# Kernel optimization log

Hardware: AMD Instinct MI355X
Metric: run time of the kernel (lower is better)

Reference implementation:

```python
import jax, jax.numpy as jnp
import numpy as np

N_NODES = 50000
N_EDGES = 1600000
N_GRAPHS = 256
F_IN = 1080   # -> 536 -> 264 -> 128 after three (k=10, s=2) convs
HID = 128
OUT = 64


def setup_inputs() -> dict:
    key = jax.random.key(0)
    ks = jax.random.split(key, 12)
    def w(k, shape, fan):
        return (jax.random.normal(k, shape, jnp.float32) / np.sqrt(fan)).astype(jnp.float32)
    x = jax.random.normal(ks[0], (N_NODES, F_IN), jnp.float32)
    edge_index = jax.random.randint(ks[1], (2, N_EDGES), 0, N_NODES, dtype=jnp.int32)
    batch = jnp.sort(jax.random.randint(ks[2], (N_NODES,), 0, N_GRAPHS, dtype=jnp.int32))
    conv_w = w(ks[3], (1, 1, 1, 10), 10)
    conv_b = jnp.zeros((1,), jnp.float32)
    W1 = w(ks[4], (HID, HID), HID); b1 = jnp.zeros((HID,), jnp.float32)
    W2 = w(ks[5], (HID, HID), HID); b2 = jnp.zeros((HID,), jnp.float32)
    W3 = w(ks[6], (HID, HID), HID); b3 = jnp.zeros((HID,), jnp.float32)
    l1w = w(ks[7], (HID, OUT), HID); l1b = jnp.zeros((OUT,), jnp.float32)
    l2w = w(ks[8], (OUT, 1), OUT);  l2b = jnp.zeros((1,), jnp.float32)
    return dict(x=x, edge_index=edge_index, batch=batch, conv_w=conv_w, conv_b=conv_b,
                W1=W1, b1=b1, W2=W2, b2=b2, W3=W3, b3=b3,
                l1w=l1w, l1b=l1b, l2w=l2w, l2b=l2b)


def reference(x, edge_index, batch, conv_w, conv_b, W1, b1, W2, b2, W3, b3, l1w, l1b, l2w, l2b):
    N = x.shape[0]
    def c2d(h):
        y = jax.lax.conv_general_dilated(h[None, None], conv_w, (1, 2), 'VALID')
        return y[0, 0] + conv_b[0]
    h = c2d(c2d(c2d(x)))  # [N, 128]

    # --- GCN normalization (self-loops + symmetric deg^-1/2) computed once ---
    loops = jnp.arange(N, dtype=edge_index.dtype)
    src = jnp.concatenate([edge_index[0], loops])
    dst = jnp.concatenate([edge_index[1], loops])
    deg = jax.ops.segment_sum(jnp.ones_like(dst, jnp.float32), dst, num_segments=N)
    dinv = jax.lax.rsqrt(jnp.maximum(deg, 1.0))  # deg >= 1 via self-loops
    norm = dinv[src] * dinv[dst]                 # [E+N]

    def gcn(h, W, b):
        m = (h @ W)[src] * norm[:, None]          # gather + scale
        return jax.ops.segment_sum(m, dst, num_segments=N) + b  # scatter-add

    h = jax.nn.relu(gcn(h, W1, b1))
    h = jax.nn.relu(gcn(h, W2, b2))
    h = gcn(h, W3, b3)                            # [N, 128]

    # --- global mean pool over graphs ---
    cnt = jax.ops.segment_sum(jnp.ones((N,), jnp.float32), batch, num_segments=N_GRAPHS)
    pooled = jax.ops.segment_sum(h, batch, num_segments=N_GRAPHS) / jnp.maximum(cnt, 1.0)[:, None]

    out = jax.nn.sigmoid(jax.nn.relu(pooled @ l1w + l1b) @ l2w + l2b)  # [256, 1]
    return out
```

## Files before the change

### kernel.cpp

```cpp
#include <hip/hip_runtime.h>

#define N_NODES 50000
#define N_PAD   50016
#define N_EDGES 1600000
#define N_GRAPHS 256
#define F_IN 1080
#define HID 128

__global__ void eff_kernel(const float* __restrict__ w, const float* __restrict__ b,
                           float* __restrict__ eff) {
  int t = threadIdx.x;
  float acc = 0.f;
  for (int a = 0; a < 10; ++a)
    for (int bb = 0; bb < 10; ++bb) {
      int r = t - a - 2 * bb;
      if (r >= 0 && (r & 3) == 0 && (r >> 2) < 10)
        acc += w[a] * w[bb] * w[r >> 2];
    }
  eff[t] = acc;
  if (t == 0) {
    float s = 0.f;
    for (int i = 0; i < 10; ++i) s += w[i];
    eff[64] = b[0] * (s * s + s + 1.f);
  }
}

__global__ __launch_bounds__(256) void conv_kernel(const float* __restrict__ x,
                                                   const float* __restrict__ eff,
                                                   float* __restrict__ h) {
  int node = blockIdx.x * 2 + (threadIdx.x >> 7);
  int f = threadIdx.x & 127;
  const float* xr = x + (size_t)node * F_IN + 8 * f;
  float acc = eff[64];
  #pragma unroll
  for (int t4 = 0; t4 < 16; ++t4) {
    float4 v = *reinterpret_cast<const float4*>(xr + 4 * t4);
    acc = fmaf(eff[4 * t4 + 0], v.x, acc);
    acc = fmaf(eff[4 * t4 + 1], v.y, acc);
    acc = fmaf(eff[4 * t4 + 2], v.z, acc);
    acc = fmaf(eff[4 * t4 + 3], v.w, acc);
  }
  h[(size_t)node * HID + f] = acc;
}

__global__ void deg_kernel(const int* __restrict__ ei, int* __restrict__ deg) {
  int e = blockIdx.x * 256 + threadIdx.x;
  if (e < N_EDGES) atomicAdd(&deg[ei[N_EDGES + e]], 1);
}

#define SCAN_B 256
#define SCAN_NB ((N_NODES + SCAN_B - 1) / SCAN_B)

__global__ void scan1_kernel(const int* __restrict__ deg, int* __restrict__ excl,
                             int* __restrict__ sums) {
  __shared__ int s[SCAN_B];
  int i = blockIdx.x * SCAN_B + threadIdx.x;
  int v = (i < N_NODES) ? deg[i] : 0;
  s[threadIdx.x] = v;
  __syncthreads();
  int val = v;
  for (int off = 1; off < SCAN_B; off <<= 1) {
    int add = (threadIdx.x >= off) ? s[threadIdx.x - off] : 0;
    __syncthreads();
    val += add;
    s[threadIdx.x] = val;
    __syncthreads();
  }
  if (i < N_NODES) excl[i] = val - v;
  if (threadIdx.x == SCAN_B - 1) sums[blockIdx.x] = val;
}

__global__ void scan2_kernel(int* __restrict__ sums) {
  __shared__ int s[SCAN_B];
  int v = (threadIdx.x < SCAN_NB) ? sums[threadIdx.x] : 0;
  s[threadIdx.x] = v;
  __syncthreads();
  int val = v;
  for (int off = 1; off < SCAN_B; off <<= 1) {
    int add = (threadIdx.x >= off) ? s[threadIdx.x - off] : 0;
    __syncthreads();
    val += add;
    s[threadIdx.x] = val;
    __syncthreads();
  }
  if (threadIdx.x < SCAN_NB) sums[threadIdx.x] = val - v;
  if (threadIdx.x == SCAN_NB - 1) sums[SCAN_NB] = val;
}

__global__ void scan3_kernel(const int* __restrict__ excl, const int* __restrict__ sums,
                             int* __restrict__ row_ptr) {
  int i = blockIdx.x * SCAN_B + threadIdx.x;
  if (i < N_NODES) row_ptr[i] = excl[i] + sums[blockIdx.x];
  if (i == 0) row_ptr[N_NODES] = sums[SCAN_NB];
}

__global__ void dinv_kernel(const int* __restrict__ deg, float* __restrict__ dinv) {
  int i = blockIdx.x * 256 + threadIdx.x;
  if (i < N_NODES) dinv[i] = rsqrtf((float)(deg[i] + 1));
}

__global__ void fill_kernel(const int* __restrict__ ei, const int* __restrict__ row_ptr,
                            int* __restrict__ fillc, const float* __restrict__ dinv,
                            int2* __restrict__ csr) {
  int e = blockIdx.x * 256 + threadIdx.x;
  if (e >= N_EDGES) return;
  int sN = ei[e], d = ei[N_EDGES + e];
  int p = atomicAdd(&fillc[d], 1);
  csr[row_ptr[d] + p] = make_int2(sN, __float_as_int(dinv[sN] * dinv[d]));
}

__global__ __launch_bounds__(256) void matmul_kernel(const float* __restrict__ h,
                                                     const float* __restrict__ W,
                                                     float* __restrict__ out) {
  int t = threadIdx.x;
  int c0 = (t & 31) << 2;
  int n0 = blockIdx.x * 32 + ((t >> 5) << 2);
  float acc[4][4];
  #pragma unroll
  for (int i = 0; i < 4; ++i)
    #pragma unroll
    for (int j = 0; j < 4; ++j) acc[i][j] = 0.f;
  for (int k = 0; k < HID; k += 4) {
    float4 w0 = *(const float4*)(W + (k + 0) * HID + c0);
    float4 w1 = *(const float4*)(W + (k + 1) * HID + c0);
    float4 w2 = *(const float4*)(W + (k + 2) * HID + c0);
    float4 w3 = *(const float4*)(W + (k + 3) * HID + c0);
    #pragma unroll
    for (int i = 0; i < 4; ++i) {
      float4 hv = *(const float4*)(h + (size_t)(n0 + i) * HID + k);
      acc[i][0] = fmaf(hv.x, w0.x, acc[i][0]); acc[i][0] = fmaf(hv.y, w1.x, acc[i][0]);
      acc[i][0] = fmaf(hv.z, w2.x, acc[i][0]); acc[i][0] = fmaf(hv.w, w3.x, acc[i][0]);
      acc[i][1] = fmaf(hv.x, w0.y, acc[i][1]); acc[i][1] = fmaf(hv.y, w1.y, acc[i][1]);
      acc[i][1] = fmaf(hv.z, w2.y, acc[i][1]); acc[i][1] = fmaf(hv.w, w3.y, acc[i][1]);
      acc[i][2] = fmaf(hv.x, w0.z, acc[i][2]); acc[i][2] = fmaf(hv.y, w1.z, acc[i][2]);
      acc[i][2] = fmaf(hv.z, w2.z, acc[i][2]); acc[i][2] = fmaf(hv.w, w3.z, acc[i][2]);
      acc[i][3] = fmaf(hv.x, w0.w, acc[i][3]); acc[i][3] = fmaf(hv.y, w1.w, acc[i][3]);
      acc[i][3] = fmaf(hv.z, w2.w, acc[i][3]); acc[i][3] = fmaf(hv.w, w3.w, acc[i][3]);
    }
  }
  #pragma unroll
  for (int i = 0; i < 4; ++i) {
    float4 r;
    r.x = acc[i][0]; r.y = acc[i][1]; r.z = acc[i][2]; r.w = acc[i][3];
    *(float4*)(out + (size_t)(n0 + i) * HID + c0) = r;
  }
}

__global__ __launch_bounds__(256) void aggregate_kernel(
    const float* __restrict__ hW, const int2* __restrict__ csr,
    const int* __restrict__ row_ptr, const float* __restrict__ dinv,
    const float* __restrict__ bias, float* __restrict__ out, int relu) {
  int v = blockIdx.x * 4 + (threadIdx.x >> 6);
  if (v >= N_NODES) return;
  int lane = threadIdx.x & 63;
  float dv = dinv[v];
  float2 hs = ((const float2*)(hW + (size_t)v * HID))[lane];
  float ax = dv * dv * hs.x, ay = dv * dv * hs.y;
  float bx = 0.f, by = 0.f;
  int beg = row_ptr[v], end = row_ptr[v + 1];
  int e = beg;
  for (; e + 1 < end; e += 2) {
    int2 e0 = csr[e];
    int2 e1 = csr[e + 1];
    float n0 = __int_as_float(e0.y);
    float n1 = __int_as_float(e1.y);
    float2 h0 = ((const float2*)(hW + (size_t)e0.x * HID))[lane];
    float2 h1 = ((const float2*)(hW + (size_t)e1.x * HID))[lane];
    ax = fmaf(n0, h0.x, ax);
    ay = fmaf(n0, h0.y, ay);
    bx = fmaf(n1, h1.x, bx);
    by = fmaf(n1, h1.y, by);
  }
  if (e < end) {
    int2 e0 = csr[e];
    float n0 = __int_as_float(e0.y);
    float2 h0 = ((const float2*)(hW + (size_t)e0.x * HID))[lane];
    ax = fmaf(n0, h0.x, ax);
    ay = fmaf(n0, h0.y, ay);
  }
  ax += bx; ay += by;
  float2 b2 = ((const float2*)bias)[lane];
  ax += b2.x; ay += b2.y;
  if (relu) { ax = fmaxf(ax, 0.f); ay = fmaxf(ay, 0.f); }
  ((float2*)(out + (size_t)v * HID))[lane] = make_float2(ax, ay);
}

#define POOL_NPB 128
__global__ __launch_bounds__(128) void pool_kernel(const float* __restrict__ h,
                                                   const int* __restrict__ batch,
                                                   float* __restrict__ pooled,
                                                   float* __restrict__ cnt) {
  int c = threadIdx.x;
  int n0 = blockIdx.x * POOL_NPB;
  int n1 = min(n0 + POOL_NPB, N_NODES);
  int g = batch[n0];
  float acc = 0.f;
  int segc = 0;
  for (int v = n0; v < n1; ++v) {
    int gv = batch[v];
    if (gv != g) {
      atomicAdd(&pooled[g * HID + c], acc);
      if (c == 0) atomicAdd(&cnt[g], (float)segc);
      acc = 0.f; segc = 0; g = gv;
    }
    acc += h[(size_t)v * HID + c];
    ++segc;
  }
  atomicAdd(&pooled[g * HID + c], acc);
  if (c == 0) atomicAdd(&cnt[g], (float)segc);
}

__global__ void mlp_kernel(const float* __restrict__ pooled, const float* __restrict__ cnt,
                           const float* __restrict__ l1w, const float* __restrict__ l1b,
                           const float* __restrict__ l2w, const float* __restrict__ l2b,
                           float* __restrict__ out) {
  int g = blockIdx.x, j = threadIdx.x;
  float inv = 1.f / fmaxf(cnt[g], 1.f);
  float acc = l1b[j];
  #pragma unroll 8
  for (int k = 0; k < HID; ++k)
    acc = fmaf(pooled[g * HID + k] * inv, l1w[k * 64 + j], acc);
  float p = fmaxf(acc, 0.f) * l2w[j];
  #pragma unroll
  for (int off = 32; off > 0; off >>= 1) p += __shfl_down(p, off, 64);
  if (j == 0) out[g] = 1.f / (1.f + __expf(-(p + l2b[0])));
}

extern "C" void kernel_launch(void* const* d_in, const int* in_sizes, int n_in,
                              void* d_out, int out_size, void* d_ws, size_t ws_size,
                              hipStream_t stream) {
  const float* x      = (const float*)d_in[0];
  const int*   ei     = (const int*)d_in[1];
  const int*   batch  = (const int*)d_in[2];
  const float* conv_w = (const float*)d_in[3];
  const float* conv_b = (const float*)d_in[4];
  const float* W1 = (const float*)d_in[5];
  const float* b1 = (const float*)d_in[6];
  const float* W2 = (const float*)d_in[7];
  const float* b2 = (const float*)d_in[8];
  const float* W3 = (const float*)d_in[9];
  const float* b3 = (const float*)d_in[10];
  const float* l1w = (const float*)d_in[11];
  const float* l1b = (const float*)d_in[12];
  const float* l2w = (const float*)d_in[13];
  const float* l2b = (const float*)d_in[14];
  float* out = (float*)d_out;

  char* ws = (char*)d_ws;
  size_t off = 0;
  auto alloc = [&](size_t bytes) {
    void* p = ws + off;
    off = (off + bytes + 255) & ~(size_t)255;
    return p;
  };
  float* hA      = (float*)alloc((size_t)N_PAD * HID * 4);
  float* hB      = (float*)alloc((size_t)N_PAD * HID * 4);
  int*   deg     = (int*)alloc((size_t)N_NODES * 4);
  int*   row_ptr = (int*)alloc((size_t)(N_NODES + 1) * 4);
  int*   fillc   = (int*)alloc((size_t)N_NODES * 4);
  float* dinv    = (float*)alloc((size_t)N_NODES * 4);
  int2*  csr     = (int2*)alloc((size_t)N_EDGES * 8);
  float* eff     = (float*)alloc(128 * 4);
  float* pooled  = (float*)alloc((size_t)N_GRAPHS * HID * 4);
  float* cnt     = (float*)alloc((size_t)N_GRAPHS * 4);
  int*   excl    = (int*)alloc((size_t)N_NODES * 4);
  int*   sums    = (int*)alloc((size_t)(SCAN_NB + 1) * 4);

  hipMemsetAsync(deg, 0, (size_t)N_NODES * 4, stream);
  hipMemsetAsync(fillc, 0, (size_t)N_NODES * 4, stream);
  hipMemsetAsync(pooled, 0, (size_t)N_GRAPHS * HID * 4, stream);
  hipMemsetAsync(cnt, 0, (size_t)N_GRAPHS * 4, stream);

  eff_kernel<<<1, 64, 0, stream>>>(conv_w, conv_b, eff);
  conv_kernel<<<N_NODES / 2, 256, 0, stream>>>(x, eff, hA);

  deg_kernel<<<(N_EDGES + 255) / 256, 256, 0, stream>>>(ei, deg);
  scan1_kernel<<<SCAN_NB, SCAN_B, 0, stream>>>(deg, excl, sums);
  scan2_kernel<<<1, SCAN_B, 0, stream>>>(sums);
  scan3_kernel<<<SCAN_NB, SCAN_B, 0, stream>>>(excl, sums, row_ptr);
  dinv_kernel<<<(N_NODES + 255) / 256, 256, 0, stream>>>(deg, dinv);
  fill_kernel<<<(N_EDGES + 255) / 256, 256, 0, stream>>>(ei, row_ptr, fillc, dinv, csr);

  matmul_kernel<<<N_PAD / 32, 256, 0, stream>>>(hA, W1, hB);
  aggregate_kernel<<<N_NODES / 4, 256, 0, stream>>>(hB, csr, row_ptr, dinv, b1, hA, 1);
  matmul_kernel<<<N_PAD / 32, 256, 0, stream>>>(hA, W2, hB);
  aggregate_kernel<<<N_NODES / 4, 256, 0, stream>>>(hB, csr, row_ptr, dinv, b2, hA, 1);
  matmul_kernel<<<N_PAD / 32, 256, 0, stream>>>(hA, W3, hB);
  aggregate_kernel<<<N_NODES / 4, 256, 0, stream>>>(hB, csr, row_ptr, dinv, b3, hA, 0);

  pool_kernel<<<(N_NODES + POOL_NPB - 1) / POOL_NPB, POOL_NPB, 0, stream>>>(hA, batch, pooled, cnt);
  mlp_kernel<<<N_GRAPHS, 64, 0, stream>>>(pooled, cnt, l1w, l1b, l2w, l2b, out);
}
```

Before: 1.063 ms.

## Store node features in bf16 and split edge aggregation across wavefront halves

Intermediate node feature buffers are now stored as bf16 with round-to-nearest-even packing, halving gather and stream traffic in the matmul, aggregate and pool kernels while accumulating in fp32. The aggregate kernel now splits each node's edges between the two 32-lane halves of a wavefront, each half loading 4 bf16 features per lane, and combines them with a cross-half shuffle. The effective-filter computation is folded into the conv kernel via shared memory, and the dinv computation is folded into the first scan kernel, removing two launches. This trades precision of the intermediates for lower memory traffic, and the per-block recomputation of the filter adds some redundant work in the conv kernel.

```diff
diff --git a/kernel.cpp b/kernel.cpp
--- a/kernel.cpp
+++ b/kernel.cpp
@@ -7,40 +7,58 @@
 #define F_IN 1080
 #define HID 128
 
-__global__ void eff_kernel(const float* __restrict__ w, const float* __restrict__ b,
-                           float* __restrict__ eff) {
-  int t = threadIdx.x;
-  float acc = 0.f;
-  for (int a = 0; a < 10; ++a)
-    for (int bb = 0; bb < 10; ++bb) {
-      int r = t - a - 2 * bb;
-      if (r >= 0 && (r & 3) == 0 && (r >> 2) < 10)
-        acc += w[a] * w[bb] * w[r >> 2];
+typedef unsigned short u16;
+typedef unsigned int u32;
+
+static __device__ __forceinline__ u32 rne(float f) {
+  u32 u = __float_as_uint(f);
+  return (u + 0x7fffu + ((u >> 16) & 1u)) >> 16;
+}
+static __device__ __forceinline__ u32 pack2(float lo, float hi) {
+  return rne(lo) | (rne(hi) << 16);
+}
+static __device__ __forceinline__ float bl(u32 u) { return __uint_as_float(u << 16); }
+static __device__ __forceinline__ float bh(u32 u) { return __uint_as_float(u & 0xffff0000u); }
+
+__global__ __launch_bounds__(256) void conv_kernel(const float* __restrict__ x,
+                                                   const float* __restrict__ w,
+                                                   const float* __restrict__ b,
+                                                   u16* __restrict__ h) {
+  __shared__ float effs[65];
+  if (threadIdx.x < 64) {
+    int t = threadIdx.x;
+    float acc = 0.f;
+    for (int a = 0; a < 10; ++a)
+      for (int bb = 0; bb < 10; ++bb) {
+        int r = t - a - 2 * bb;
+        if (r >= 0 && (r & 3) == 0 && (r >> 2) < 10)
+          acc += w[a] * w[bb] * w[r >> 2];
+      }
+    effs[t] = acc;
+    if (t == 0) {
+      float s = 0.f;
+      for (int i = 0; i < 10; ++i) s += w[i];
+      effs[64] = b[0] * (s * s + s + 1.f);
     }
-  eff[t] = acc;
-  if (t == 0) {
-    float s = 0.f;
-    for (int i = 0; i < 10; ++i) s += w[i];
-    eff[64] = b[0] * (s * s + s + 1.f);
-  }
-}
-
-__global__ __launch_bounds__(256) void conv_kernel(const float* __restrict__ x,
-                                                   const float* __restrict__ eff,
-                                                   float* __restrict__ h) {
+  }
+  __syncthreads();
   int node = blockIdx.x * 2 + (threadIdx.x >> 7);
   int f = threadIdx.x & 127;
+  if (node >= N_NODES) {
+    if (node < N_PAD) h[(size_t)node * HID + f] = 0;
+    return;
+  }
   const float* xr = x + (size_t)node * F_IN + 8 * f;
-  float acc = eff[64];
+  float acc = effs[64];
   #pragma unroll
   for (int t4 = 0; t4 < 16; ++t4) {
     float4 v = *reinterpret_cast<const float4*>(xr + 4 * t4);
-    acc = fmaf(eff[4 * t4 + 0], v.x, acc);
-    acc = fmaf(eff[4 * t4 + 1], v.y, acc);
-    acc = fmaf(eff[4 * t4 + 2], v.z, acc);
-    acc = fmaf(eff[4 * t4 + 3], v.w, acc);
-  }
-  h[(size_t)node * HID + f] = acc;
+    acc = fmaf(effs[4 * t4 + 0], v.x, acc);
+    acc = fmaf(effs[4 * t4 + 1], v.y, acc);
+    acc = fmaf(effs[4 * t4 + 2], v.z, acc);
+    acc = fmaf(effs[4 * t4 + 3], v.w, acc);
+  }
+  h[(size_t)node * HID + f] = (u16)rne(acc);
 }
 
 __global__ void deg_kernel(const int* __restrict__ ei, int* __restrict__ deg) {
@@ -52,10 +70,11 @@
 #define SCAN_NB ((N_NODES + SCAN_B - 1) / SCAN_B)
 
 __global__ void scan1_kernel(const int* __restrict__ deg, int* __restrict__ excl,
-                             int* __restrict__ sums) {
+                             int* __restrict__ sums, float* __restrict__ dinv) {
   __shared__ int s[SCAN_B];
   int i = blockIdx.x * SCAN_B + threadIdx.x;
   int v = (i < N_NODES) ? deg[i] : 0;
+  if (i < N_NODES) dinv[i] = rsqrtf((float)(v + 1));
   s[threadIdx.x] = v;
   __syncthreads();
   int val = v;
@@ -94,11 +113,6 @@
   if (i == 0) row_ptr[N_NODES] = sums[SCAN_NB];
 }
 
-__global__ void dinv_kernel(const int* __restrict__ deg, float* __restrict__ dinv) {
-  int i = blockIdx.x * 256 + threadIdx.x;
-  if (i < N_NODES) dinv[i] = rsqrtf((float)(deg[i] + 1));
-}
-
 __global__ void fill_kernel(const int* __restrict__ ei, const int* __restrict__ row_ptr,
                             int* __restrict__ fillc, const float* __restrict__ dinv,
                             int2* __restrict__ csr) {
@@ -109,9 +123,9 @@
   csr[row_ptr[d] + p] = make_int2(sN, __float_as_int(dinv[sN] * dinv[d]));
 }
 
-__global__ __launch_bounds__(256) void matmul_kernel(const float* __restrict__ h,
+__global__ __launch_bounds__(256) void matmul_kernel(const u16* __restrict__ h,
                                                      const float* __restrict__ W,
-                                                     float* __restrict__ out) {
+                                                     u16* __restrict__ out) {
   int t = threadIdx.x;
   int c0 = (t & 31) << 2;
   int n0 = blockIdx.x * 32 + ((t >> 5) << 2);
@@ -127,66 +141,77 @@
     float4 w3 = *(const float4*)(W + (k + 3) * HID + c0);
     #pragma unroll
     for (int i = 0; i < 4; ++i) {
-      float4 hv = *(const float4*)(h + (size_t)(n0 + i) * HID + k);
-      acc[i][0] = fmaf(hv.x, w0.x, acc[i][0]); acc[i][0] = fmaf(hv.y, w1.x, acc[i][0]);
-      acc[i][0] = fmaf(hv.z, w2.x, acc[i][0]); acc[i][0] = fmaf(hv.w, w3.x, acc[i][0]);
-      acc[i][1] = fmaf(hv.x, w0.y, acc[i][1]); acc[i][1] = fmaf(hv.y, w1.y, acc[i][1]);
-      acc[i][1] = fmaf(hv.z, w2.y, acc[i][1]); acc[i][1] = fmaf(hv.w, w3.y, acc[i][1]);
-      acc[i][2] = fmaf(hv.x, w0.z, acc[i][2]); acc[i][2] = fmaf(hv.y, w1.z, acc[i][2]);
-      acc[i][2] = fmaf(hv.z, w2.z, acc[i][2]); acc[i][2] = fmaf(hv.w, w3.z, acc[i][2]);
-      acc[i][3] = fmaf(hv.x, w0.w, acc[i][3]); acc[i][3] = fmaf(hv.y, w1.w, acc[i][3]);
-      acc[i][3] = fmaf(hv.z, w2.w, acc[i][3]); acc[i][3] = fmaf(hv.w, w3.w, acc[i][3]);
+      uint2 hu = *(const uint2*)(h + (size_t)(n0 + i) * HID + k);
+      float f0 = bl(hu.x), f1 = bh(hu.x), f2 = bl(hu.y), f3 = bh(hu.y);
+      acc[i][0] = fmaf(f0, w0.x, acc[i][0]); acc[i][0] = fmaf(f1, w1.x, acc[i][0]);
+      acc[i][0] = fmaf(f2, w2.x, acc[i][0]); acc[i][0] = fmaf(f3, w3.x, acc[i][0]);
+      acc[i][1] = fmaf(f0, w0.y, acc[i][1]); acc[i][1] = fmaf(f1, w1.y, acc[i][1]);
+      acc[i][1] = fmaf(f2, w2.y, acc[i][1]); acc[i][1] = fmaf(f3, w3.y, acc[i][1]);
+      acc[i][2] = fmaf(f0, w0.z, acc[i][2]); acc[i][2] = fmaf(f1, w1.z, acc[i][2]);
+      acc[i][2] = fmaf(f2, w2.z, acc[i][2]); acc[i][2] = fmaf(f3, w3.z, acc[i][2]);
+      acc[i][3] = fmaf(f0, w0.w, acc[i][3]); acc[i][3] = fmaf(f1, w1.w, acc[i][3]);
+      acc[i][3] = fmaf(f2, w2.w, acc[i][3]); acc[i][3] = fmaf(f3, w3.w, acc[i][3]);
     }
   }
   #pragma unroll
   for (int i = 0; i < 4; ++i) {
-    float4 r;
-    r.x = acc[i][0]; r.y = acc[i][1]; r.z = acc[i][2]; r.w = acc[i][3];
-    *(float4*)(out + (size_t)(n0 + i) * HID + c0) = r;
+    uint2 o;
+    o.x = pack2(acc[i][0], acc[i][1]);
+    o.y = pack2(acc[i][2], acc[i][3]);
+    *(uint2*)(out + (size_t)(n0 + i) * HID + c0) = o;
   }
 }
 
 __global__ __launch_bounds__(256) void aggregate_kernel(
-    const float* __restrict__ hW, const int2* __restrict__ csr,
+    const u16* __restrict__ hW, const int2* __restrict__ csr,
     const int* __restrict__ row_ptr, const float* __restrict__ dinv,
-    const float* __restrict__ bias, float* __restrict__ out, int relu) {
+    const float* __restrict__ bias, u16* __restrict__ out, int relu) {
   int v = blockIdx.x * 4 + (threadIdx.x >> 6);
   if (v >= N_NODES) return;
   int lane = threadIdx.x & 63;
+  int half = lane >> 5, li = lane & 31;
   float dv = dinv[v];
-  float2 hs = ((const float2*)(hW + (size_t)v * HID))[lane];
-  float ax = dv * dv * hs.x, ay = dv * dv * hs.y;
-  float bx = 0.f, by = 0.f;
+  float sw = (half == 0) ? dv * dv : 0.f;
+  uint2 sv = ((const uint2*)(hW + (size_t)v * HID))[li];
+  float a0 = sw * bl(sv.x), a1 = sw * bh(sv.x), a2 = sw * bl(sv.y), a3 = sw * bh(sv.y);
+  float b0 = 0.f, b1 = 0.f, b2 = 0.f, b3 = 0.f;
   int beg = row_ptr[v], end = row_ptr[v + 1];
-  int e = beg;
-  for (; e + 1 < end; e += 2) {
+  int e = beg + half;
+  for (; e + 2 < end; e += 4) {
     int2 e0 = csr[e];
-    int2 e1 = csr[e + 1];
-    float n0 = __int_as_float(e0.y);
-    float n1 = __int_as_float(e1.y);
-    float2 h0 = ((const float2*)(hW + (size_t)e0.x * HID))[lane];
-    float2 h1 = ((const float2*)(hW + (size_t)e1.x * HID))[lane];
-    ax = fmaf(n0, h0.x, ax);
-    ay = fmaf(n0, h0.y, ay);
-    bx = fmaf(n1, h1.x, bx);
-    by = fmaf(n1, h1.y, by);
+    int2 e1 = csr[e + 2];
+    uint2 g0 = ((const uint2*)(hW + (size_t)e0.x * HID))[li];
+    uint2 g1 = ((const uint2*)(hW + (size_t)e1.x * HID))[li];
+    float n0 = __int_as_float(e0.y), n1 = __int_as_float(e1.y);
+    a0 = fmaf(n0, bl(g0.x), a0); a1 = fmaf(n0, bh(g0.x), a1);
+    a2 = fmaf(n0, bl(g0.y), a2); a3 = fmaf(n0, bh(g0.y), a3);
+    b0 = fmaf(n1, bl(g1.x), b0); b1 = fmaf(n1, bh(g1.x), b1);
+    b2 = fmaf(n1, bl(g1.y), b2); b3 = fmaf(n1, bh(g1.y), b3);
   }
   if (e < end) {
     int2 e0 = csr[e];
+    uint2 g0 = ((const uint2*)(hW + (size_t)e0.x * HID))[li];
     float n0 = __int_as_float(e0.y);
-    float2 h0 = ((const float2*)(hW + (size_t)e0.x * HID))[lane];
-    ax = fmaf(n0, h0.x, ax);
-    ay = fmaf(n0, h0.y, ay);
-  }
-  ax += bx; ay += by;
-  float2 b2 = ((const float2*)bias)[lane];
-  ax += b2.x; ay += b2.y;
-  if (relu) { ax = fmaxf(ax, 0.f); ay = fmaxf(ay, 0.f); }
-  ((float2*)(out + (size_t)v * HID))[lane] = make_float2(ax, ay);
+    a0 = fmaf(n0, bl(g0.x), a0); a1 = fmaf(n0, bh(g0.x), a1);
+    a2 = fmaf(n0, bl(g0.y), a2); a3 = fmaf(n0, bh(g0.y), a3);
+  }
+  a0 += b0; a1 += b1; a2 += b2; a3 += b3;
+  a0 += __shfl_xor(a0, 32); a1 += __shfl_xor(a1, 32);
+  a2 += __shfl_xor(a2, 32); a3 += __shfl_xor(a3, 32);
+  if (half == 0) {
+    float4 bv = *(const float4*)(bias + 4 * li);
+    a0 += bv.x; a1 += bv.y; a2 += bv.z; a3 += bv.w;
+    if (relu) {
+      a0 = fmaxf(a0, 0.f); a1 = fmaxf(a1, 0.f);
+      a2 = fmaxf(a2, 0.f); a3 = fmaxf(a3, 0.f);
+    }
+    uint2 o; o.x = pack2(a0, a1); o.y = pack2(a2, a3);
+    ((uint2*)(out + (size_t)v * HID))[li] = o;
+  }
 }
 
 #define POOL_NPB 128
-__global__ __launch_bounds__(128) void pool_kernel(const float* __restrict__ h,
+__global__ __launch_bounds__(128) void pool_kernel(const u16* __restrict__ h,
                                                    const int* __restrict__ batch,
                                                    float* __restrict__ pooled,
                                                    float* __restrict__ cnt) {
@@ -203,7 +228,7 @@
       if (c == 0) atomicAdd(&cnt[g], (float)segc);
       acc = 0.f; segc = 0; g = gv;
     }
-    acc += h[(size_t)v * HID + c];
+    acc += bl((u32)h[(size_t)v * HID + c]);
     ++segc;
   }
   atomicAdd(&pooled[g * HID + c], acc);
@@ -253,14 +278,13 @@
     off = (off + bytes + 255) & ~(size_t)255;
     return p;
   };
-  float* hA      = (float*)alloc((size_t)N_PAD * HID * 4);
-  float* hB      = (float*)alloc((size_t)N_PAD * HID * 4);
+  u16*   B0      = (u16*)alloc((size_t)N_PAD * HID * 2);
+  u16*   B1      = (u16*)alloc((size_t)N_PAD * HID * 2);
   int*   deg     = (int*)alloc((size_t)N_NODES * 4);
   int*   row_ptr = (int*)alloc((size_t)(N_NODES + 1) * 4);
   int*   fillc   = (int*)alloc((size_t)N_NODES * 4);
   float* dinv    = (float*)alloc((size_t)N_NODES * 4);
   int2*  csr     = (int2*)alloc((size_t)N_EDGES * 8);
-  float* eff     = (float*)alloc(128 * 4);
   float* pooled  = (float*)alloc((size_t)N_GRAPHS * HID * 4);
   float* cnt     = (float*)alloc((size_t)N_GRAPHS * 4);
   int*   excl    = (int*)alloc((size_t)N_NODES * 4);
@@ -271,23 +295,21 @@
   hipMemsetAsync(pooled, 0, (size_t)N_GRAPHS * HID * 4, stream);
   hipMemsetAsync(cnt, 0, (size_t)N_GRAPHS * 4, stream);
 
-  eff_kernel<<<1, 64, 0, stream>>>(conv_w, conv_b, eff);
-  conv_kernel<<<N_NODES / 2, 256, 0, stream>>>(x, eff, hA);
+  conv_kernel<<<N_PAD / 2, 256, 0, stream>>>(x, conv_w, conv_b, B0);
 
   deg_kernel<<<(N_EDGES + 255) / 256, 256, 0, stream>>>(ei, deg);
-  scan1_kernel<<<SCAN_NB, SCAN_B, 0, stream>>>(deg, excl, sums);
+  scan1_kernel<<<SCAN_NB, SCAN_B, 0, stream>>>(deg, excl, sums, dinv);
   scan2_kernel<<<1, SCAN_B, 0, stream>>>(sums);
   scan3_kernel<<<SCAN_NB, SCAN_B, 0, stream>>>(excl, sums, row_ptr);
-  dinv_kernel<<<(N_NODES + 255) / 256, 256, 0, stream>>>(deg, dinv);
   fill_kernel<<<(N_EDGES + 255) / 256, 256, 0, stream>>>(ei, row_ptr, fillc, dinv, csr);
 
-  matmul_kernel<<<N_PAD / 32, 256, 0, stream>>>(hA, W1, hB);
-  aggregate_kernel<<<N_NODES / 4, 256, 0, stream>>>(hB, csr, row_ptr, dinv, b1, hA, 1);
-  matmul_kernel<<<N_PAD / 32, 256, 0, stream>>>(hA, W2, hB);
-  aggregate_kernel<<<N_NODES / 4, 256, 0, stream>>>(hB, csr, row_ptr, dinv, b2, hA, 1);
-  matmul_kernel<<<N_PAD / 32, 256, 0, stream>>>(hA, W3, hB);
-  aggregate_kernel<<<N_NODES / 4, 256, 0, stream>>>(hB, csr, row_ptr, dinv, b3, hA, 0);
-
-  pool_kernel<<<(N_NODES + POOL_NPB - 1) / POOL_NPB, POOL_NPB, 0, stream>>>(hA, batch, pooled, cnt);
+  matmul_kernel<<<N_PAD / 32, 256, 0, stream>>>(B0, W1, B1);
+  aggregate_kernel<<<N_NODES / 4, 256, 0, stream>>>(B1, csr, row_ptr, dinv, b1, B0, 1);
+  matmul_kernel<<<N_PAD / 32, 256, 0, stream>>>(B0, W2, B1);
+  aggregate_kernel<<<N_NODES / 4, 256, 0, stream>>>(B1, csr, row_ptr, dinv, b2, B0, 1);
+  matmul_kernel<<<N_PAD / 32, 256, 0, stream>>>(B0, W3, B1);
+  aggregate_kernel<<<N_NODES / 4, 256, 0, stream>>>(B1, csr, row_ptr, dinv, b3, B0, 0);
+
+  pool_kernel<<<(N_NODES + POOL_NPB - 1) / POOL_NPB, POOL_NPB, 0, stream>>>(B0, batch, pooled, cnt);
   mlp_kernel<<<N_GRAPHS, 64, 0, stream>>>(pooled, cnt, l1w, l1b, l2w, l2b, out);
 }
```

Measured after the change: 994.3 us. -6.4%, faster.
